# Performance work log

Hardware: AMD Instinct MI355X
Metric: run time of the kernel (lower is better)

The kernel has to match this reference:

```python
import jax, jax.numpy as jnp
import numpy as np
import functools

N_NODES = 16
WIDTH = 64
C_DIM = 3
LATENT_DIM = 8
B = 131072


def build_graph(n=N_NODES, k=4, p=0.75, seed=0):
    """Watts-Strogatz-style random graph oriented low->high node id (DAG),
    mirroring build_random_graph(nodes, 1 input, 1 output, p=0.75, k=4)."""
    rng = np.random.RandomState(seed)
    edges = set()
    for i in range(n):
        for d in range(1, k // 2 + 1):
            j = (i + d) % n
            if rng.rand() < p:
                j = int(rng.randint(n))
            a, b = min(i, j), max(i, j)
            if a != b:
                edges.add((a, b))
    preds = [set() for _ in range(n)]
    for a, b in edges:
        preds[b].add(a)
    # every non-source node must have a predecessor (connectivity)
    for j in range(1, n):
        if not preds[j]:
            a = int(rng.randint(j))
            preds[j].add(a)
            edges.add((a, j))
    succs = [set() for _ in range(n)]
    for a, b in edges:
        succs[a].add(b)
    preds = [sorted(p_) for p_ in preds]
    sources = [j for j in range(n) if not preds[j]]   # receive the INR feature f
    sinks = [j for j in range(n) if not succs[j]]     # combined into the single output
    return preds, sources, sinks


def gaussian(x):
    return jnp.exp(-0.5 * x * x)

# 'large' activation set for graph nodes, assigned deterministically per node
GRAPH_ACTS = [jnp.tanh, jax.nn.elu, jax.nn.softplus, jnp.sin, gaussian]


def setup_inputs() -> dict:
    key = jax.random.key(0)
    ks = jax.random.split(key, 16)

    def nrm(k, shape, s):
        return jax.random.normal(k, shape, dtype=jnp.float32) * s

    inputs = jax.random.normal(ks[0], (B, 3, 1), dtype=jnp.float32)   # (x, y, r) coords
    latents = jax.random.normal(ks[1], (B, LATENT_DIM), dtype=jnp.float32)
    Wl = nrm(ks[2], (WIDTH, LATENT_DIM), 0.3)
    bl = jnp.zeros((WIDTH,), jnp.float32)
    Wx = nrm(ks[3], (WIDTH, 1), 1.0)
    Wy = nrm(ks[4], (WIDTH, 1), 1.0)
    Wr = nrm(ks[5], (WIDTH, 1), 1.0)
    W1 = nrm(ks[6], (WIDTH, WIDTH), 0.15)
    b1 = jnp.zeros((WIDTH,), jnp.float32)
    gW = nrm(ks[7], (N_NODES, WIDTH, WIDTH), 0.15)   # per-graph-node Linear(width,width)
    gB = jnp.zeros((N_NODES, WIDTH), jnp.float32)
    outW = nrm(ks[8], (C_DIM, WIDTH), 0.15)          # combine -> c_dim output
    outb = jnp.zeros((C_DIM,), jnp.float32)
    scale = jnp.ones((1,), jnp.float32)              # ScaleAct learnable scalar
    return {"inputs": inputs, "latents": latents, "Wl": Wl, "bl": bl, "Wx": Wx,
            "Wy": Wy, "Wr": Wr, "W1": W1, "b1": b1, "gW": gW, "gB": gB,
            "outW": outW, "outb": outb, "scale": scale}


def reference(inputs, latents, Wl, bl, Wx, Wy, Wr, W1, b1, gW, gB, outW, outb, scale):
    x, y, r = inputs[:, 0, :], inputs[:, 1, :], inputs[:, 2, :]   # each (B, 1)
    latents_ = jnp.tanh(latents @ Wl.T + bl)      # acts_start[0] = Tanh
    r_ = jax.nn.elu(r @ Wr.T)                     # acts_start[1] = ELU
    y_ = jax.nn.softplus(y @ Wy.T)                # acts_start[2] = Softplus
    x_ = jnp.tanh(x @ Wx.T)                       # acts_start[3] = Tanh
    f = gaussian(x_ + y_ + r_ + latents_)         # acts_start[4] = Gaussian
    f = jnp.sin(f @ W1.T + b1)                    # acts_start[5] = SinLayer

    # random-topology graph network: gather(sum preds) -> linear -> activation
    preds, sources, sinks = build_graph()
    hs = []
    for j in range(N_NODES):
        if j in sources:
            inp = f
        else:
            inp = functools.reduce(lambda a, b_: a + b_, [hs[i] for i in preds[j]])
        hs.append(GRAPH_ACTS[j % len(GRAPH_ACTS)](inp @ gW[j].T + gB[j]))
    agg = functools.reduce(lambda a, b_: a + b_, [hs[j] for j in sinks])
    res = (agg @ outW.T + outb) * scale           # combine + ScaleAct
    return jax.nn.sigmoid(res)                    # final_activation='sigmoid'
```

## Files before the change

### kernel.cpp

```cpp
#include <hip/hip_runtime.h>
#include <cstdint>

#define NN 16
#define W64 64
#define MT 64
#define NSTAGE 17
#define IST 72
#define WST 72

typedef _Float16 half8   __attribute__((ext_vector_type(8)));
typedef _Float16 half16  __attribute__((ext_vector_type(16)));
typedef float    floatx4 __attribute__((ext_vector_type(4)));

struct GPlan {
    unsigned pred[NN];
    unsigned sinkmask;
    int slot[NSTAGE];
    int nslot;
};

constexpr unsigned mt_next(unsigned (&mt)[624], int &mti) {
    if (mti >= 624) {
        for (int i = 0; i < 624; ++i) {
            const unsigned y = (mt[i] & 0x80000000u) | (mt[(i + 1) % 624] & 0x7fffffffu);
            unsigned v = mt[(i + 397) % 624] ^ (y >> 1);
            if (y & 1u) v ^= 0x9908b0dfu;
            mt[i] = v;
        }
        mti = 0;
    }
    unsigned y = mt[mti++];
    y ^= y >> 11;
    y ^= (y << 7)  & 0x9d2c5680u;
    y ^= (y << 15) & 0xefc60000u;
    y ^= y >> 18;
    return y;
}
constexpr double mt_rnd(unsigned (&mt)[624], int &mti) {
    const unsigned a = mt_next(mt, mti) >> 5;
    const unsigned b = mt_next(mt, mti) >> 6;
    return (a * 67108864.0 + b) / 9007199254740992.0;
}
constexpr long mt_randint(unsigned (&mt)[624], int &mti, long n) {
    const unsigned long maxv = (unsigned long)n - 1;
    if (maxv == 0) return 0;
    unsigned long mask = maxv;
    mask |= mask >> 1;  mask |= mask >> 2;  mask |= mask >> 4;
    mask |= mask >> 8;  mask |= mask >> 16;
    unsigned long v = (unsigned long)mt_next(mt, mti) & mask;
    while (v > maxv) v = (unsigned long)mt_next(mt, mti) & mask;
    return (long)v;
}

constexpr GPlan build_plan() {
    GPlan P = {};
    unsigned mt[624] = {};
    mt[0] = 0u;
    for (int i = 1; i < 624; ++i)
        mt[i] = 1812433253u * (mt[i-1] ^ (mt[i-1] >> 30)) + (unsigned)i;
    int mti = 624;

    bool edge[NN][NN] = {};
    for (int i = 0; i < NN; ++i) {
        for (int d = 1; d <= 2; ++d) {
            int j = (i + d) & (NN - 1);
            if (mt_rnd(mt, mti) < 0.75) j = (int)mt_randint(mt, mti, NN);
            const int a = i < j ? i : j;
            const int b = i < j ? j : i;
            if (a != b) edge[a][b] = true;
        }
    }
    for (int a = 0; a < NN; ++a)
        for (int b = 0; b < NN; ++b)
            if (edge[a][b]) P.pred[b] |= 1u << a;
    for (int j = 1; j < NN; ++j) {
        if (!P.pred[j]) {
            const int a = (int)mt_randint(mt, mti, j);
            P.pred[j] |= 1u << a;
            edge[a][j] = true;
        }
    }
    unsigned succ[NN] = {};
    for (int a = 0; a < NN; ++a)
        for (int b = 0; b < NN; ++b)
            if (edge[a][b]) succ[a] |= 1u << b;
    for (int j = 0; j < NN; ++j)
        if (!succ[j]) P.sinkmask |= 1u << j;

    int lastuse[NSTAGE] = {};
    for (int v = 0; v < NSTAGE; ++v) lastuse[v] = -1;
    for (int j = 0; j < NN; ++j) {
        const unsigned pm = P.pred[j];
        if (pm == 0u) { if (j > lastuse[16]) lastuse[16] = j; }
        else for (int i = 0; i < NN; ++i)
            if (pm & (1u << i)) { if (j > lastuse[i]) lastuse[i] = j; }
    }
    for (int i = 0; i < NN; ++i)
        if (P.sinkmask & (1u << i)) lastuse[i] = 17;

    int defstage[NSTAGE] = {};
    for (int i = 0; i < NN; ++i) defstage[i] = i + 1;
    defstage[16] = 0;

    int nmax = 0;
    for (int s = 0; s <= 16; ++s) {
        const int w = (s == 0) ? 16 : (s - 1);
        bool busy[NSTAGE] = {};
        for (int v = 0; v < NSTAGE; ++v) {
            if (v == w) continue;
            if (defstage[v] < s && lastuse[v] >= s)
                busy[P.slot[v]] = true;
        }
        int k = 0;
        while (busy[k]) ++k;
        P.slot[w] = k;
        if (k + 1 > nmax) nmax = k + 1;
    }
    P.nslot = nmax;
    return P;
}

constexpr GPlan kPlan = build_plan();
constexpr int NSLOT = kPlan.nslot;

__device__ __forceinline__ float act_tanh(float x)     { return 1.0f - 2.0f / (1.0f + __expf(2.0f * x)); }
__device__ __forceinline__ float act_elu(float x)      { return x > 0.0f ? x : __expf(x) - 1.0f; }
__device__ __forceinline__ float act_softplus(float x) { return fmaxf(x, 0.0f) + __logf(1.0f + __expf(-fabsf(x))); }
__device__ __forceinline__ float act_gauss(float x)    { return __expf(-0.5f * x * x); }

__device__ __forceinline__ float apply_act(int a, float x) {
    switch (a) {
        case 0:  return act_tanh(x);
        case 1:  return act_elu(x);
        case 2:  return act_softplus(x);
        case 3:  return __sinf(x);
        default: return act_gauss(x);
    }
}

__device__ __forceinline__ half8 cvt8(float4 a, float4 b) {
    half8 h;
    h[0]=(_Float16)a.x; h[1]=(_Float16)a.y; h[2]=(_Float16)a.z; h[3]=(_Float16)a.w;
    h[4]=(_Float16)b.x; h[5]=(_Float16)b.y; h[6]=(_Float16)b.z; h[7]=(_Float16)b.w;
    return h;
}

__global__ __launch_bounds__(256, 3) void inr_mfma_kernel(
    const float* __restrict__ inputs, const float* __restrict__ latents,
    const float* __restrict__ Wl, const float* __restrict__ bl,
    const float* __restrict__ Wx, const float* __restrict__ Wy,
    const float* __restrict__ Wr, const float* __restrict__ W1,
    const float* __restrict__ b1, const float* __restrict__ gW,
    const float* __restrict__ gB, const float* __restrict__ outW,
    const float* __restrict__ outb, const float* __restrict__ scale,
    float* __restrict__ out, int Btot)
{
    __shared__ __align__(16) _Float16 inpbuf[2][MT * IST];
    __shared__ __align__(16) _Float16 wbuf[2][W64 * WST];

    const int tid  = threadIdx.x;
    const int lane = tid & 63;
    const int wv   = tid >> 6;
    const int q    = lane >> 4;
    const int c    = lane & 15;
    const int rowbase = wv * 16;
    const int m0   = blockIdx.x * MT;

    const int srow = tid >> 3;
    const int sc8  = tid & 7;

    half16 hreg[NSLOT];

    {
        const int em = tid >> 2, ep = tid & 3;
        int mg = m0 + em; if (mg >= Btot) mg = Btot - 1;
        const float x = inputs[mg * 3 + 0];
        const float y = inputs[mg * 3 + 1];
        const float r = inputs[mg * 3 + 2];
        const float4 l0 = *(const float4*)(latents + mg * 8);
        const float4 l1 = *(const float4*)(latents + mg * 8 + 4);
        #pragma unroll
        for (int i = 0; i < 16; ++i) {
            const int k = ep * 16 + i;
            const float4 a = *(const float4*)(Wl + k * 8);
            const float4 b = *(const float4*)(Wl + k * 8 + 4);
            float ld = bl[k];
            ld = fmaf(l0.x, a.x, ld); ld = fmaf(l0.y, a.y, ld);
            ld = fmaf(l0.z, a.z, ld); ld = fmaf(l0.w, a.w, ld);
            ld = fmaf(l1.x, b.x, ld); ld = fmaf(l1.y, b.y, ld);
            ld = fmaf(l1.z, b.z, ld); ld = fmaf(l1.w, b.w, ld);
            const float tk = act_tanh(x * Wx[k]) + act_softplus(y * Wy[k])
                           + act_elu(r * Wr[k]) + act_tanh(ld);
            inpbuf[0][em * IST + k] = (_Float16)act_gauss(tk);
        }
    }
    {
        const float4* src = (const float4*)W1;
        const float4 f0 = src[2 * tid],       f1 = src[2 * tid + 1];
        const float4 f2 = src[2 * tid + 512], f3 = src[2 * tid + 513];
        *(half8*)&wbuf[0][srow * WST + sc8 * 8]        = cvt8(f0, f1);
        *(half8*)&wbuf[0][(srow + 32) * WST + sc8 * 8] = cvt8(f2, f3);
    }
    __syncthreads();

    #pragma unroll
    for (int s = 0; s < NSTAGE; ++s) {
        const int slot = s & 1;

        float4 nf0, nf1, nf2, nf3;
        if (s + 1 < NSTAGE) {
            const float4* src = (const float4*)(gW + s * 4096);
            nf0 = src[2 * tid];       nf1 = src[2 * tid + 1];
            nf2 = src[2 * tid + 512]; nf3 = src[2 * tid + 513];
        }

        const half8 a0 = *(const half8*)&inpbuf[slot][(rowbase + c) * IST +  0 + q * 8];
        const half8 a1 = *(const half8*)&inpbuf[slot][(rowbase + c) * IST + 32 + q * 8];

        floatx4 acc[4];
        #pragma unroll
        for (int t = 0; t < 4; ++t) {
            const half8 b0  = *(const half8*)&wbuf[slot][(t * 16 + c) * WST +  0 + q * 8];
            const half8 b1f = *(const half8*)&wbuf[slot][(t * 16 + c) * WST + 32 + q * 8];
            floatx4 z = {0.f, 0.f, 0.f, 0.f};
            z = __builtin_amdgcn_mfma_f32_16x16x32_f16(a0, b0, z, 0, 0, 0);
            z = __builtin_amdgcn_mfma_f32_16x16x32_f16(a1, b1f, z, 0, 0, 0);
            acc[t] = z;
        }

        const float* bias = (s == 0) ? b1 : (gB + (s - 1) * W64);
        const int an    = (s == 0) ? 3 : ((s - 1) % 5);
        const int hslot = kPlan.slot[(s == 0) ? 16 : (s - 1)];
        #pragma unroll
        for (int t = 0; t < 4; ++t) {
            const float bs = bias[t * 16 + c];
            #pragma unroll
            for (int r = 0; r < 4; ++r) {
                const float v = apply_act(an, acc[t][r] + bs);
                hreg[hslot][t * 4 + r] = (_Float16)v;
            }
        }

        if (s + 1 < NSTAGE) {
            const unsigned pm = kPlan.pred[s];
            half16 sum;
            if (pm == 0u) {
                sum = hreg[kPlan.slot[16]];
            } else {
                #pragma unroll
                for (int v = 0; v < 16; ++v) sum[v] = (_Float16)0.0f;
                #pragma unroll
                for (int i = 0; i < NN; ++i) {
                    if (pm & (1u << i)) {
                        sum += hreg[kPlan.slot[i]];
                    }
                }
            }
            const int wslot = (s + 1) & 1;
            #pragma unroll
            for (int t = 0; t < 4; ++t)
                #pragma unroll
                for (int r = 0; r < 4; ++r)
                    inpbuf[wslot][(rowbase + q * 4 + r) * IST + t * 16 + c] =
                        sum[t * 4 + r];
            *(half8*)&wbuf[wslot][srow * WST + sc8 * 8]        = cvt8(nf0, nf1);
            *(half8*)&wbuf[wslot][(srow + 32) * WST + sc8 * 8] = cvt8(nf2, nf3);
        }
        __syncthreads();
    }

    {
        half16 sum;
        #pragma unroll
        for (int v = 0; v < 16; ++v) sum[v] = (_Float16)0.0f;
        #pragma unroll
        for (int j = 0; j < NN; ++j) {
            if (kPlan.sinkmask & (1u << j)) {
                sum += hreg[kPlan.slot[j]];
            }
        }
        #pragma unroll
        for (int t = 0; t < 4; ++t)
            #pragma unroll
            for (int r = 0; r < 4; ++r)
                inpbuf[1][(rowbase + q * 4 + r) * IST + t * 16 + c] = sum[t * 4 + r];
    }
    __syncthreads();
    {
        const int em = tid >> 2, ep = tid & 3;
        float p0 = 0.f, p1 = 0.f, p2 = 0.f;
        #pragma unroll
        for (int h = 0; h < 2; ++h) {
            const half8 hv = *(const half8*)&inpbuf[1][em * IST + ep * 16 + h * 8];
            #pragma unroll
            for (int i = 0; i < 8; ++i) {
                const float av = (float)hv[i];
                const int k = ep * 16 + h * 8 + i;
                p0 = fmaf(av, outW[0 * W64 + k], p0);
                p1 = fmaf(av, outW[1 * W64 + k], p1);
                p2 = fmaf(av, outW[2 * W64 + k], p2);
            }
        }
        p0 += __shfl_xor(p0, 1); p0 += __shfl_xor(p0, 2);
        p1 += __shfl_xor(p1, 1); p1 += __shfl_xor(p1, 2);
        p2 += __shfl_xor(p2, 1); p2 += __shfl_xor(p2, 2);
        const int mg = m0 + em;
        if (ep < 3 && mg < Btot) {
            const float pr = (ep == 0) ? p0 : ((ep == 1) ? p1 : p2);
            const float res = (pr + outb[ep]) * scale[0];
            out[mg * 3 + ep] = 1.0f / (1.0f + __expf(-res));
        }
    }
}

extern "C" void kernel_launch(void* const* d_in, const int* in_sizes, int n_in,
                              void* d_out, int out_size, void* d_ws, size_t ws_size,
                              hipStream_t stream)
{
    const float* inputs  = (const float*)d_in[0];
    const float* latents = (const float*)d_in[1];
    const float* Wl      = (const float*)d_in[2];
    const float* bl      = (const float*)d_in[3];
    const float* Wx      = (const float*)d_in[4];
    const float* Wy      = (const float*)d_in[5];
    const float* Wr      = (const float*)d_in[6];
    const float* W1      = (const float*)d_in[7];
    const float* b1      = (const float*)d_in[8];
    const float* gW      = (const float*)d_in[9];
    const float* gB      = (const float*)d_in[10];
    const float* outW    = (const float*)d_in[11];
    const float* outb    = (const float*)d_in[12];
    const float* scale   = (const float*)d_in[13];
    float* out = (float*)d_out;

    const int Btot = in_sizes[0] / 3;
    const int blocks = (Btot + MT - 1) / MT;
    inr_mfma_kernel<<<blocks, 256, 0, stream>>>(
        inputs, latents, Wl, bl, Wx, Wy, Wr, W1, b1, gW, gB, outW, outb, scale,
        out, Btot);
}
```

Baseline: 194.4 us.

## Read pre-converted fp16 weights from global and drop LDS weight staging and barriers

A small pre-kernel converts W1 and all graph weights to fp16 in workspace. The main kernel then has each wave load its MFMA B-operands straight from global memory (L1/L2 cached) instead of staging weights through double-buffered LDS. Because each wave's activation rows in LDS are now only touched by that same wave, the per-stage block barriers are removed. The bias is also folded into the accumulator initialisation. The trade-off is that weight loads are no longer prefetched a stage ahead, so their global latency may sit on the critical path, and there is an extra kernel launch.

```diff
diff --git a/kernel.cpp b/kernel.cpp
--- a/kernel.cpp
+++ b/kernel.cpp
@@ -6,7 +6,6 @@
 #define MT 64
 #define NSTAGE 17
 #define IST 72
-#define WST 72
 
 typedef _Float16 half8   __attribute__((ext_vector_type(8)));
 typedef _Float16 half16  __attribute__((ext_vector_type(16)));
@@ -145,6 +144,17 @@
     return h;
 }
 
+__global__ void convert_weights(const float* __restrict__ W1,
+                                const float* __restrict__ gW,
+                                _Float16* __restrict__ ws)
+{
+    const int i = blockIdx.x * 256 + threadIdx.x;
+    if (i >= NSTAGE * 4096) return;
+    const float v = (i < 4096) ? W1[i] : gW[i - 4096];
+    ws[i] = (_Float16)v;
+}
+
+template<bool F16W>
 __global__ __launch_bounds__(256, 3) void inr_mfma_kernel(
     const float* __restrict__ inputs, const float* __restrict__ latents,
     const float* __restrict__ Wl, const float* __restrict__ bl,
@@ -153,10 +163,10 @@
     const float* __restrict__ b1, const float* __restrict__ gW,
     const float* __restrict__ gB, const float* __restrict__ outW,
     const float* __restrict__ outb, const float* __restrict__ scale,
+    const _Float16* __restrict__ wsW,
     float* __restrict__ out, int Btot)
 {
     __shared__ __align__(16) _Float16 inpbuf[2][MT * IST];
-    __shared__ __align__(16) _Float16 wbuf[2][W64 * WST];
 
     const int tid  = threadIdx.x;
     const int lane = tid & 63;
@@ -165,9 +175,6 @@
     const int c    = lane & 15;
     const int rowbase = wv * 16;
     const int m0   = blockIdx.x * MT;
-
-    const int srow = tid >> 3;
-    const int sc8  = tid & 7;
 
     half16 hreg[NSLOT];
 
@@ -194,49 +201,45 @@
             inpbuf[0][em * IST + k] = (_Float16)act_gauss(tk);
         }
     }
-    {
-        const float4* src = (const float4*)W1;
-        const float4 f0 = src[2 * tid],       f1 = src[2 * tid + 1];
-        const float4 f2 = src[2 * tid + 512], f3 = src[2 * tid + 513];
-        *(half8*)&wbuf[0][srow * WST + sc8 * 8]        = cvt8(f0, f1);
-        *(half8*)&wbuf[0][(srow + 32) * WST + sc8 * 8] = cvt8(f2, f3);
-    }
-    __syncthreads();
 
     #pragma unroll
     for (int s = 0; s < NSTAGE; ++s) {
         const int slot = s & 1;
 
-        float4 nf0, nf1, nf2, nf3;
-        if (s + 1 < NSTAGE) {
-            const float4* src = (const float4*)(gW + s * 4096);
-            nf0 = src[2 * tid];       nf1 = src[2 * tid + 1];
-            nf2 = src[2 * tid + 512]; nf3 = src[2 * tid + 513];
-        }
-
         const half8 a0 = *(const half8*)&inpbuf[slot][(rowbase + c) * IST +  0 + q * 8];
         const half8 a1 = *(const half8*)&inpbuf[slot][(rowbase + c) * IST + 32 + q * 8];
 
+        const float* bias = (s == 0) ? b1 : (gB + (s - 1) * W64);
         floatx4 acc[4];
         #pragma unroll
         for (int t = 0; t < 4; ++t) {
-            const half8 b0  = *(const half8*)&wbuf[slot][(t * 16 + c) * WST +  0 + q * 8];
-            const half8 b1f = *(const half8*)&wbuf[slot][(t * 16 + c) * WST + 32 + q * 8];
-            floatx4 z = {0.f, 0.f, 0.f, 0.f};
+            half8 b0, b1f;
+            if constexpr (F16W) {
+                const _Float16* wrow = wsW + (s * 64 + t * 16 + c) * 64;
+                b0  = *(const half8*)(wrow + q * 8);
+                b1f = *(const half8*)(wrow + 32 + q * 8);
+            } else {
+                const float* wrow = ((s == 0) ? W1 : (gW + (s - 1) * 4096))
+                                  + (t * 16 + c) * 64;
+                b0  = cvt8(*(const float4*)(wrow + q * 8),
+                           *(const float4*)(wrow + q * 8 + 4));
+                b1f = cvt8(*(const float4*)(wrow + 32 + q * 8),
+                           *(const float4*)(wrow + 32 + q * 8 + 4));
+            }
+            const float bs = bias[t * 16 + c];
+            floatx4 z = {bs, bs, bs, bs};
             z = __builtin_amdgcn_mfma_f32_16x16x32_f16(a0, b0, z, 0, 0, 0);
             z = __builtin_amdgcn_mfma_f32_16x16x32_f16(a1, b1f, z, 0, 0, 0);
             acc[t] = z;
         }
 
-        const float* bias = (s == 0) ? b1 : (gB + (s - 1) * W64);
         const int an    = (s == 0) ? 3 : ((s - 1) % 5);
         const int hslot = kPlan.slot[(s == 0) ? 16 : (s - 1)];
         #pragma unroll
         for (int t = 0; t < 4; ++t) {
-            const float bs = bias[t * 16 + c];
             #pragma unroll
             for (int r = 0; r < 4; ++r) {
-                const float v = apply_act(an, acc[t][r] + bs);
+                const float v = apply_act(an, acc[t][r]);
                 hreg[hslot][t * 4 + r] = (_Float16)v;
             }
         }
@@ -263,10 +266,7 @@
                 for (int r = 0; r < 4; ++r)
                     inpbuf[wslot][(rowbase + q * 4 + r) * IST + t * 16 + c] =
                         sum[t * 4 + r];
-            *(half8*)&wbuf[wslot][srow * WST + sc8 * 8]        = cvt8(nf0, nf1);
-            *(half8*)&wbuf[wslot][(srow + 32) * WST + sc8 * 8] = cvt8(nf2, nf3);
-        }
-        __syncthreads();
+        }
     }
 
     {
@@ -285,7 +285,6 @@
             for (int r = 0; r < 4; ++r)
                 inpbuf[1][(rowbase + q * 4 + r) * IST + t * 16 + c] = sum[t * 4 + r];
     }
-    __syncthreads();
     {
         const int em = tid >> 2, ep = tid & 3;
         float p0 = 0.f, p1 = 0.f, p2 = 0.f;
@@ -335,7 +334,17 @@
 
     const int Btot = in_sizes[0] / 3;
     const int blocks = (Btot + MT - 1) / MT;
-    inr_mfma_kernel<<<blocks, 256, 0, stream>>>(
-        inputs, latents, Wl, bl, Wx, Wy, Wr, W1, b1, gW, gB, outW, outb, scale,
-        out, Btot);
-}
+    const size_t wbytes = (size_t)NSTAGE * 4096 * sizeof(_Float16);
+
+    if (ws_size >= wbytes) {
+        _Float16* wsW = (_Float16*)d_ws;
+        convert_weights<<<(NSTAGE * 4096 + 255) / 256, 256, 0, stream>>>(W1, gW, wsW);
+        inr_mfma_kernel<true><<<blocks, 256, 0, stream>>>(
+            inputs, latents, Wl, bl, Wx, Wy, Wr, W1, b1, gW, gB, outW, outb, scale,
+            wsW, out, Btot);
+    } else {
+        inr_mfma_kernel<false><<<blocks, 256, 0, stream>>>(
+            inputs, latents, Wl, bl, Wx, Wy, Wr, W1, b1, gW, gB, outW, outb, scale,
+            (const _Float16*)nullptr, out, Btot);
+    }
+}
```

Result: slower. 368.5 us (+89.5%).
